# Kernel tuning notes

Hardware: AMD Instinct MI355X
Metric: run time of the kernel (lower is better)

Reference implementation:

```python
import jax, jax.numpy as jnp
import numpy as np

B, T, C, L = 1024, 256, 128, 64
NEG = -1e30  # finite stand-in for -inf (safe gradients)
EPS = 1e-7   # keras.backend.epsilon()


def setup_inputs() -> dict:
    key = jax.random.key(0)
    k1, k2 = jax.random.split(key)
    # y_pred is a softmax output (probabilities), as keras ctc_batch_cost expects
    logits = jax.random.normal(k1, (B, T, C), dtype=jnp.float32)
    y_pred = jax.nn.softmax(logits, axis=-1)
    # labels in [0, C-2]; class C-1 is the CTC blank (keras convention)
    y_true = jax.random.randint(k2, (B, L), 0, C - 1, dtype=jnp.int64)
    return {"y_true": y_true, "y_pred": y_pred}


def ctc_loss(y_true, y_pred):
    """Negative log-likelihood CTC loss per sample, shape [B, 1].
    Matches keras.backend.ctc_batch_cost with full input/label lengths,
    blank index = num_classes - 1, log(y_pred + eps)."""
    Bb, Tt, Cc = y_pred.shape
    Ll = y_true.shape[1]
    blank = Cc - 1
    S = 2 * Ll + 1  # extended label: blank, l1, blank, l2, ..., blank

    logp = jnp.log(y_pred + EPS)  # [B, T, C]

    ext = jnp.full((Bb, S), blank, dtype=y_true.dtype).at[:, 1::2].set(y_true)  # [B, S]
    # per-(t, s) log-prob of the extended symbol: lp[b, t, s] = logp[b, t, ext[b, s]]
    lp = jnp.take_along_axis(logp, ext[:, None, :], axis=2)  # [B, T, S]

    # skip transition s-2 -> s allowed iff ext[s] != blank and ext[s] != ext[s-2]
    ext_m2 = jnp.concatenate(
        [jnp.full((Bb, 2), blank, dtype=ext.dtype), ext[:, :-2]], axis=1)
    can_skip = (ext != blank) & (ext != ext_m2)  # [B, S]

    def shift1(a):
        return jnp.concatenate(
            [jnp.full((Bb, 1), NEG, dtype=a.dtype), a[:, :-1]], axis=1)

    # alpha init at t=0: only s=0 (blank) and s=1 (first label) reachable
    alpha0 = (jnp.full((Bb, S), NEG, dtype=lp.dtype)
              .at[:, 0].set(lp[:, 0, 0])
              .at[:, 1].set(lp[:, 0, 1]))

    def step(alpha, lp_t):
        a1 = shift1(alpha)
        a2 = jnp.where(can_skip, shift1(shift1(alpha)), NEG)
        new = jax.nn.logsumexp(jnp.stack([alpha, a1, a2], axis=0), axis=0) + lp_t
        return new, None

    lp_tbs = jnp.swapaxes(lp, 0, 1)  # [T, B, S]
    alpha, _ = jax.lax.scan(step, alpha0, lp_tbs[1:])

    log_lik = jnp.logaddexp(alpha[:, S - 1], alpha[:, S - 2])  # end on last blank or last label
    return -log_lik[:, None]  # [B, 1], matching ctc_batch_cost output shape


def reference(y_true, y_pred):
    return ctc_loss(y_true, y_pred)
```

## Files before the change

kernel.cpp:

```cpp
#include <hip/hip_runtime.h>
#include <math.h>


#define Bn 1024
#define Tn 256
#define Cn 128
#define Ln 64
#define BLANK 127
#define U 8
#define NC (Tn / U)
#define RING 8
#define DEPTH 7
#define EPS128 (1e-7f * 128.0f)
#define LN2 0.69314718055994530942f

#define WAIT_VM(n) __builtin_amdgcn_s_waitcnt((((n) & 0xF) | (((n) >> 4) << 14)) | 0x0F70)
#define SCHED_FENCE() __builtin_amdgcn_sched_barrier(0)

template <int CTRL>
__device__ __forceinline__ float dpp_movf(float x) {
    return __int_as_float(__builtin_amdgcn_update_dpp(
        0, __float_as_int(x), CTRL, 0xF, 0xF, true));
}
__device__ __forceinline__ int dpp_shr1_i(int x) {
    return __builtin_amdgcn_update_dpp(0, x, 0x138, 0xF, 0xF, true);
}
__device__ __forceinline__ void dma16(const float* g, float* l) {
    __builtin_amdgcn_global_load_lds(
        (const __attribute__((address_space(1))) void*)g,
        (__attribute__((address_space(3))) void*)l, 16, 0, 0);
}

__global__ __launch_bounds__(64)
void ctc_ring_kernel(const int* __restrict__ y_true,
                     const float* __restrict__ y_pred,
                     float* __restrict__ out) {
    __shared__ __align__(16) float ring[RING][U * Cn];
    const int b = blockIdx.x;
    const int i = threadIdx.x;

    const int li = y_true[b * Ln + i];
    const int ll = dpp_shr1_i(li);
    const float skf = (li != ll) ? 1.0f : 0.0f;

    const float* gb = y_pred + (size_t)b * (Tn * Cn);

    auto issue_chunk = [&](int c) {
        const float* g = gb + c * (U * Cn);
        float* l = ring[c & (RING - 1)];
#pragma unroll
        for (int k = 0; k < 4; ++k)
            dma16(g + k * 256 + i * 4, l + k * 256);
    };

    float qlA[U], qbA[U], qlB[U], qbB[U];
    auto qread = [&](int c, float* ql, float* qb) {
        const float* s = ring[c & (RING - 1)];
#pragma unroll
        for (int j = 0; j < U; ++j) {
            ql[j] = fmaf(s[j * Cn + li],    128.0f, EPS128);
            qb[j] = fmaf(s[j * Cn + BLANK], 128.0f, EPS128);
        }
    };

    float E = 0.f, O = 0.f, X = 0.f;
    int Esum = 0;

    auto steps = [&](const float* ql, const float* qb, bool first) {
#pragma unroll
        for (int j = 0; j < U; ++j) {
            if (first && j == 0) {
                E = (i == 0) ? qb[0] : 0.f;
                O = (i == 0) ? ql[0] : 0.f;
                X = 0.f;
                continue;
            }
            const float Ol = dpp_movf<0x138>(O);
            const float t1 = O + E;
            const float nO = fmaf(skf, Ol, t1) * ql[j];
            const float nE = (E + Ol) * qb[j];
            const float nX = (X + O) * qb[j];
            E = nE; O = nO; X = nX;
        }
    };
    auto renorm = [&]() {
        float m = fmaxf(E, O);
        if (i == 63) m = fmaxf(m, X);
        m = fmaxf(m, dpp_movf<0x111>(m));
        m = fmaxf(m, dpp_movf<0x112>(m));
        m = fmaxf(m, dpp_movf<0x114>(m));
        m = fmaxf(m, dpp_movf<0x118>(m));
        m = fmaxf(m, dpp_movf<0x142>(m));
        m = fmaxf(m, dpp_movf<0x143>(m));
        const unsigned ub =
            (unsigned)__builtin_amdgcn_readlane(__float_as_int(m), 63);
        const int eb = (int)(ub >> 23);
        const float sc = __int_as_float((unsigned)(254 - eb) << 23);
        Esum += eb - 127;
        E *= sc; O *= sc; X *= sc;
    };

#pragma unroll
    for (int c = 0; c < DEPTH; ++c) issue_chunk(c);
    WAIT_VM(24);
    SCHED_FENCE();
    qread(0, qlA, qbA);

    for (int cc = 0; cc < 24; cc += 2) {
        WAIT_VM(20); SCHED_FENCE();
        qread(cc + 1, qlB, qbB);
        issue_chunk(cc + 7);
        steps(qlA, qbA, cc == 0);
        renorm();
        WAIT_VM(20); SCHED_FENCE();
        qread(cc + 2, qlA, qbA);
        issue_chunk(cc + 8);
        steps(qlB, qbB, false);
        renorm();
    }
    WAIT_VM(20); SCHED_FENCE();
    qread(25, qlB, qbB);
    issue_chunk(31);
    steps(qlA, qbA, false);
    renorm();
    WAIT_VM(0); SCHED_FENCE();
    qread(26, qlA, qbA);
    steps(qlB, qbB, false);
    renorm();
    qread(27, qlB, qbB); steps(qlA, qbA, false); renorm();
    qread(28, qlA, qbA); steps(qlB, qbB, false); renorm();
    qread(29, qlB, qbB); steps(qlA, qbA, false); renorm();
    qread(30, qlA, qbA); steps(qlB, qbB, false); renorm();
    qread(31, qlB, qbB); steps(qlA, qbA, false); renorm();
    steps(qlB, qbB, false);

    if (i == 63) {
        const float s = O + X;
#if __has_builtin(__builtin_amdgcn_logf)
        const float l2 = __builtin_amdgcn_logf(s);
#else
        const float l2 = log2f(s);
#endif
        out[b] = -(l2 + (float)(Esum - 7 * Tn)) * LN2;
    }
}

extern "C" void kernel_launch(void* const* d_in, const int* in_sizes, int n_in,
                              void* d_out, int out_size, void* d_ws, size_t ws_size,
                              hipStream_t stream) {
    const int*   y_true = (const int*)d_in[0];
    const float* y_pred = (const float*)d_in[1];
    float*       out    = (float*)d_out;
    hipLaunchKernelGGL(ctc_ring_kernel, dim3(Bn), dim3(64), 0, stream,
                       y_true, y_pred, out);
}
```

Before: 192.1 us.

## Replace LDS ring DMA with register-resident prefetch and bpermute gather

Drops the global_load_lds ring buffer in shared memory. Each chunk is now loaded straight into per-thread float4 registers, with a 14-chunk prefetch depth. The per-label probability is gathered across lanes with ds_bpermute plus selects, and the blank probability comes from readlane. The loop is fully unrolled and relies on compiler-inserted waits instead of manual waitcnt. This removes LDS staging but adds heavy register pressure (56 float4s), four bpermutes per step, and possibly coarser memory waits.

```diff
diff --git a/kernel.cpp b/kernel.cpp
--- a/kernel.cpp
+++ b/kernel.cpp
@@ -8,13 +8,11 @@
 #define Ln 64
 #define BLANK 127
 #define U 8
-#define NC (Tn / U)
-#define RING 8
-#define DEPTH 7
+#define NCH (Tn / U)
+#define DEPTH 14
 #define EPS128 (1e-7f * 128.0f)
 #define LN2 0.69314718055994530942f
 
-#define WAIT_VM(n) __builtin_amdgcn_s_waitcnt((((n) & 0xF) | (((n) >> 4) << 14)) | 0x0F70)
 #define SCHED_FENCE() __builtin_amdgcn_sched_barrier(0)
 
 template <int CTRL>
@@ -25,41 +23,52 @@
 __device__ __forceinline__ int dpp_shr1_i(int x) {
     return __builtin_amdgcn_update_dpp(0, x, 0x138, 0xF, 0xF, true);
 }
-__device__ __forceinline__ void dma16(const float* g, float* l) {
-    __builtin_amdgcn_global_load_lds(
-        (const __attribute__((address_space(1))) void*)g,
-        (__attribute__((address_space(3))) void*)l, 16, 0, 0);
-}
 
 __global__ __launch_bounds__(64)
-void ctc_ring_kernel(const int* __restrict__ y_true,
-                     const float* __restrict__ y_pred,
-                     float* __restrict__ out) {
-    __shared__ __align__(16) float ring[RING][U * Cn];
+void ctc_reg_kernel(const int* __restrict__ y_true,
+                    const float* __restrict__ y_pred,
+                    float* __restrict__ out) {
     const int b = blockIdx.x;
     const int i = threadIdx.x;
 
     const int li = y_true[b * Ln + i];
     const int ll = dpp_shr1_i(li);
     const float skf = (li != ll) ? 1.0f : 0.0f;
+    const bool sel0 = (li & 1) != 0;
+    const bool sel1 = (li & 2) != 0;
+    const int idx0 = (li >> 2) << 2;
 
     const float* gb = y_pred + (size_t)b * (Tn * Cn);
 
-    auto issue_chunk = [&](int c) {
+    float4 buf[DEPTH][4];
+
+    auto issue = [&](int c) {
+        const int s = c % DEPTH;
         const float* g = gb + c * (U * Cn);
-        float* l = ring[c & (RING - 1)];
 #pragma unroll
         for (int k = 0; k < 4; ++k)
-            dma16(g + k * 256 + i * 4, l + k * 256);
+            buf[s][k] = *reinterpret_cast<const float4*>(g + k * 256 + i * 4);
     };
 
-    float qlA[U], qbA[U], qlB[U], qbB[U];
-    auto qread = [&](int c, float* ql, float* qb) {
-        const float* s = ring[c & (RING - 1)];
+    auto gatherq = [&](int c, float* ql, float* qb) {
+        const int s = c % DEPTH;
 #pragma unroll
         for (int j = 0; j < U; ++j) {
-            ql[j] = fmaf(s[j * Cn + li],    128.0f, EPS128);
-            qb[j] = fmaf(s[j * Cn + BLANK], 128.0f, EPS128);
+            const int k = j >> 1;
+            const int h = j & 1;
+            const int sl4 = idx0 + (h << 7);
+            const float4 v = buf[s][k];
+            const int a0 = __builtin_amdgcn_ds_bpermute(sl4, __float_as_int(v.x));
+            const int a1 = __builtin_amdgcn_ds_bpermute(sl4, __float_as_int(v.y));
+            const int a2 = __builtin_amdgcn_ds_bpermute(sl4, __float_as_int(v.z));
+            const int a3 = __builtin_amdgcn_ds_bpermute(sl4, __float_as_int(v.w));
+            const float g01 = sel0 ? __int_as_float(a1) : __int_as_float(a0);
+            const float g23 = sel0 ? __int_as_float(a3) : __int_as_float(a2);
+            const float g = sel1 ? g23 : g01;
+            ql[j] = fmaf(g, 128.0f, EPS128);
+            const float bl = __int_as_float(
+                __builtin_amdgcn_readlane(__float_as_int(v.w), 31 + (h << 5)));
+            qb[j] = fmaf(bl, 128.0f, EPS128);
         }
     };
 
@@ -101,38 +110,23 @@
     };
 
 #pragma unroll
-    for (int c = 0; c < DEPTH; ++c) issue_chunk(c);
-    WAIT_VM(24);
+    for (int c = 0; c < DEPTH; ++c) issue(c);
     SCHED_FENCE();
-    qread(0, qlA, qbA);
 
-    for (int cc = 0; cc < 24; cc += 2) {
-        WAIT_VM(20); SCHED_FENCE();
-        qread(cc + 1, qlB, qbB);
-        issue_chunk(cc + 7);
-        steps(qlA, qbA, cc == 0);
-        renorm();
-        WAIT_VM(20); SCHED_FENCE();
-        qread(cc + 2, qlA, qbA);
-        issue_chunk(cc + 8);
-        steps(qlB, qbB, false);
-        renorm();
+    float qlv[2][U], qbv[2][U];
+    gatherq(0, qlv[0], qbv[0]);
+
+#pragma unroll
+    for (int cc = 0; cc < NCH; ++cc) {
+        if (cc + DEPTH < NCH) {
+            issue(cc + DEPTH);
+            SCHED_FENCE();
+        }
+        if (cc + 1 < NCH)
+            gatherq(cc + 1, qlv[(cc + 1) & 1], qbv[(cc + 1) & 1]);
+        steps(qlv[cc & 1], qbv[cc & 1], cc == 0);
+        if (cc != NCH - 1) renorm();
     }
-    WAIT_VM(20); SCHED_FENCE();
-    qread(25, qlB, qbB);
-    issue_chunk(31);
-    steps(qlA, qbA, false);
-    renorm();
-    WAIT_VM(0); SCHED_FENCE();
-    qread(26, qlA, qbA);
-    steps(qlB, qbB, false);
-    renorm();
-    qread(27, qlB, qbB); steps(qlA, qbA, false); renorm();
-    qread(28, qlA, qbA); steps(qlB, qbB, false); renorm();
-    qread(29, qlB, qbB); steps(qlA, qbA, false); renorm();
-    qread(30, qlA, qbA); steps(qlB, qbB, false); renorm();
-    qread(31, qlB, qbB); steps(qlA, qbA, false); renorm();
-    steps(qlB, qbB, false);
 
     if (i == 63) {
         const float s = O + X;
@@ -151,6 +145,6 @@
     const int*   y_true = (const int*)d_in[0];
     const float* y_pred = (const float*)d_in[1];
     float*       out    = (float*)d_out;
-    hipLaunchKernelGGL(ctc_ring_kernel, dim3(Bn), dim3(64), 0, stream,
+    hipLaunchKernelGGL(ctc_reg_kernel, dim3(Bn), dim3(64), 0, stream,
                        y_true, y_pred, out);
 }
```

After: 198.1 us. +3.1%, slower.
